# Kernel optimization log

Measured on AMD Instinct MI355X. Metric: run time of the kernel, lower is better.

Reference implementation:

```python
import jax, jax.numpy as jnp
import numpy as np

N_NODES = 100000
N_EDGES = 3200000
FEAT = 32
N_ITER = 6  # -> n_iter - 1 = 5 SimpleConv layers
MIN_VAL, MAX_VAL = 0.0, 2.0


def setup_inputs() -> dict:
    key = jax.random.key(0)
    k = jax.random.split(key, 6)
    return {
        "x": jax.random.uniform(k[0], (N_NODES, FEAT), dtype=jnp.float32) * 2.0,
        "edge_index": jax.random.randint(k[1], (2, N_EDGES), 0, N_NODES, dtype=jnp.int32),
        "edge_mask": jax.random.randint(k[2], (N_EDGES,), 0, 2, dtype=jnp.int32),
        "edge_scale": jax.random.uniform(k[3], (N_EDGES,), dtype=jnp.float32),
        "pert_mask": jax.random.uniform(k[4], (N_EDGES,), dtype=jnp.float32),
        "edge_weight": jax.random.uniform(k[5], (N_EDGES,), dtype=jnp.float32),
    }


def reference(x, edge_index, edge_mask, edge_scale, pert_mask, edge_weight):
    # edge_index *= edge_mask (masked edges collapse to node 0, as in the torch code)
    ei = edge_index * edge_mask.astype(edge_index.dtype)  # [2, E]
    src, dst = ei[0], ei[1]
    # edge_weight = (edge_weight * (1 - pert_mask) + pert_mask) * edge_scale
    w = (edge_weight * (1.0 - pert_mask) + pert_mask) * edge_scale  # [E]

    def step(x, _):
        # SimpleConv(aggr='sum'): out[dst] += w_e * x[src]
        msgs = x[src] * w[:, None]                                   # [E, F]
        x_new = jax.ops.segment_sum(msgs, dst, num_segments=N_NODES)  # [N, F]
        # max_update: x + Hardtanh(-1,1)(x_new - x)
        x_new = x + jnp.clip(x_new - x, -1.0, 1.0)
        # act: Hardtanh(min_val, max_val)
        return jnp.clip(x_new, MIN_VAL, MAX_VAL), None

    x, _ = jax.lax.scan(step, x, None, length=N_ITER - 1)
    return x
```

## Files before the change

### kernel.cpp

```cpp
#include <hip/hip_runtime.h>
#include <hip/hip_fp16.h>

#define NNODES 100000
#define NEDGES 3200000
#define FEAT 32
#define NITER 5
#define NF (NNODES * FEAT)

#define BUCK_SH 8
#define BUCK_SZ 256
#define NBK 391
#define CHUNKF 4096
#define NBF 782
#define NT (NBF * NBK)
#define NTB 299

__global__ void ws_kernel(const int* __restrict__ edge_index,
                          const int* __restrict__ edge_mask,
                          const float* __restrict__ edge_scale,
                          const float* __restrict__ pert_mask,
                          const float* __restrict__ edge_weight,
                          int2* __restrict__ pay,
                          unsigned short* __restrict__ bkt,
                          int* __restrict__ M,
                          float* __restrict__ S_part) {
    __shared__ int h[NBK];
    __shared__ float sred[256];
    const int b = blockIdx.x;
    for (int k = threadIdx.x; k < NBK; k += 256) h[k] = 0;
    __syncthreads();
    const int base = b * CHUNKF;
    float ms = 0.0f;
    for (int it = 0; it < CHUNKF / 256; ++it) {
        const int e = base + it * 256 + threadIdx.x;
        if (e < NEDGES) {
            const int m = edge_mask[e];
            const float w = (edge_weight[e] * (1.0f - pert_mask[e]) + pert_mask[e]) * edge_scale[e];
            const int src = edge_index[e];
            const int dst = edge_index[NEDGES + e];
            pay[e] = make_int2(src | ((dst & (BUCK_SZ - 1)) << 20), __float_as_int(w));
            if (m) {
                bkt[e] = (unsigned short)(dst >> BUCK_SH);
                atomicAdd(&h[dst >> BUCK_SH], 1);
            } else {
                bkt[e] = (unsigned short)0xFFFFu;
                ms += w;
            }
        }
    }
    sred[threadIdx.x] = ms;
    __syncthreads();
    for (int off = 128; off; off >>= 1) {
        if (threadIdx.x < off) sred[threadIdx.x] += sred[threadIdx.x + off];
        __syncthreads();
    }
    if (threadIdx.x == 0) S_part[b] = sred[0];
    for (int k = threadIdx.x; k < NBK; k += 256) M[b * NBK + k] = h[k];
}

__global__ void sreduce_kernel(const float* __restrict__ S_part, float* __restrict__ S) {
    __shared__ float s[1024];
    float a = 0.0f;
    for (int i = threadIdx.x; i < NBF; i += 1024) a += S_part[i];
    s[threadIdx.x] = a;
    __syncthreads();
    for (int off = 512; off; off >>= 1) {
        if (threadIdx.x < off) s[threadIdx.x] += s[threadIdx.x + off];
        __syncthreads();
    }
    if (threadIdx.x == 0) *S = s[0];
}

__global__ void tscan1_kernel(const int* __restrict__ M, int* __restrict__ tb) {
    __shared__ int s[1024];
    const int i = blockIdx.x * 1024 + threadIdx.x;
    int v = 0;
    if (i < NT) v = M[(i % NBF) * NBK + (i / NBF)];
    s[threadIdx.x] = v;
    __syncthreads();
    for (int off = 512; off; off >>= 1) {
        if (threadIdx.x < off) s[threadIdx.x] += s[threadIdx.x + off];
        __syncthreads();
    }
    if (threadIdx.x == 0) tb[blockIdx.x] = s[0];
}

__global__ void tscan2_kernel(const int* __restrict__ tb, int* __restrict__ tboff,
                              int* __restrict__ bucket_base) {
    __shared__ int s[512];
    const int tid = threadIdx.x;
    int v = (tid < NTB) ? tb[tid] : 0;
    s[tid] = v;
    __syncthreads();
    for (int off = 1; off < 512; off <<= 1) {
        int t = (tid >= off) ? s[tid - off] : 0;
        __syncthreads();
        s[tid] += t;
        __syncthreads();
    }
    if (tid < NTB) tboff[tid] = s[tid] - v;
    if (tid == 511) bucket_base[NBK] = s[511];
}

__global__ void tscan3_kernel(const int* __restrict__ M, const int* __restrict__ tboff,
                              int* __restrict__ scanT, int* __restrict__ bucket_base) {
    __shared__ int s[1024];
    const int tid = threadIdx.x;
    const int i = blockIdx.x * 1024 + tid;
    int v = 0;
    if (i < NT) v = M[(i % NBF) * NBK + (i / NBF)];
    s[tid] = v;
    __syncthreads();
    for (int off = 1; off < 1024; off <<= 1) {
        int t = (tid >= off) ? s[tid - off] : 0;
        __syncthreads();
        s[tid] += t;
        __syncthreads();
    }
    if (i < NT) {
        const int excl = tboff[blockIdx.x] + s[tid] - v;
        scanT[i] = excl;
        if (i % NBF == 0) bucket_base[i / NBF] = excl;
    }
}

__global__ void fill782_kernel(const int2* __restrict__ pay,
                               const unsigned short* __restrict__ bkt,
                               const int* __restrict__ scanT,
                               int2* __restrict__ e8tmp) {
    __shared__ int off[NBK];
    const int b = blockIdx.x;
    for (int k = threadIdx.x; k < NBK; k += 256) off[k] = scanT[k * NBF + b];
    __syncthreads();
    const int base = b * CHUNKF;
    for (int it = 0; it < CHUNKF / 256; ++it) {
        const int e = base + it * 256 + threadIdx.x;
        if (e < NEDGES) {
            const unsigned short k = bkt[e];
            if (k != 0xFFFFu) {
                const int pos = atomicAdd(&off[k], 1);
                e8tmp[pos] = pay[e];
            }
        }
    }
}

__global__ void bsort_kernel(const int2* __restrict__ e8tmp,
                             const int* __restrict__ bucket_base,
                             unsigned* __restrict__ e4,
                             int* __restrict__ row_ptr) {
    __shared__ int h[BUCK_SZ];
    __shared__ int s[BUCK_SZ];
    __shared__ int woff[BUCK_SZ];
    const int k = blockIdx.x;
    const int tid = threadIdx.x;
    const int base0 = bucket_base[k];
    const int cnt = bucket_base[k + 1] - base0;
    h[tid] = 0;
    __syncthreads();
    for (int i = tid; i < cnt; i += 256) {
        const int dstl = e8tmp[base0 + i].x >> 20;
        atomicAdd(&h[dstl], 1);
    }
    __syncthreads();
    s[tid] = h[tid];
    __syncthreads();
    for (int off = 1; off < BUCK_SZ; off <<= 1) {
        int t = (tid >= off) ? s[tid - off] : 0;
        __syncthreads();
        s[tid] += t;
        __syncthreads();
    }
    {
        const int excl = s[tid] - h[tid];
        const int d = k * BUCK_SZ + tid;
        if (d < NNODES) row_ptr[d] = base0 + excl;
        woff[tid] = excl;
    }
    if (k == NBK - 1 && tid == 0) row_ptr[NNODES] = bucket_base[NBK];
    __syncthreads();
    for (int i = tid; i < cnt; i += 256) {
        const int2 v = e8tmp[base0 + i];
        const int dstl = v.x >> 20;
        const unsigned src = (unsigned)(v.x & 0xFFFFF);
        __half hw = __float2half_rn(__int_as_float(v.y));
        const unsigned h16 = (unsigned)(*reinterpret_cast<unsigned short*>(&hw)) & 0x7FFFu;
        const int pos = atomicAdd(&woff[dstl], 1);
        e4[base0 + pos] = (src << 15) | h16;
    }
}

__global__ void cvt_kernel(const float* __restrict__ x, __half* __restrict__ xh) {
    const int i = blockIdx.x * 256 + threadIdx.x;
    const float4 v = reinterpret_cast<const float4*>(x)[i];
    const int node = i >> 3;
    const int q = i & 7;
    const int fh = q >> 2;
    const int part = q & 3;
    __half2 h01 = __floats2half2_rn(v.x, v.y);
    __half2 h23 = __floats2half2_rn(v.z, v.w);
    *reinterpret_cast<uint2*>((char*)xh + (size_t)fh * (NNODES * 32) + node * 32 + part * 8)
        = make_uint2(*(unsigned*)&h01, *(unsigned*)&h23);
}

__global__ void gather_kernel(const __half* __restrict__ xh,
                              const int* __restrict__ row_ptr,
                              const unsigned* __restrict__ e4,
                              const float* __restrict__ S,
                              float* __restrict__ out,
                              __half* __restrict__ outh) {
    const int bid = blockIdx.x;
    const int r = bid & 7;
    const int fh = r >> 2;
    const int blk = (bid >> 3) * 4 + (r & 3);
    if (blk >= 6250) return;
    const int lane = threadIdx.x & 63;
    const int wid = threadIdx.x >> 6;
    const int nq   = lane >> 4;
    const int slot = (lane >> 1) & 7;
    const int part = lane & 1;
    const int node = blk * 16 + wid * 4 + nq;
    const int beg = row_ptr[node];
    const int end = row_ptr[node + 1];
    const char* xhc = (const char*)xh + (size_t)fh * (NNODES * 32);

    float a0=0.f,a1=0.f,a2=0.f,a3=0.f,a4=0.f,a5=0.f,a6=0.f,a7=0.f;
    const int em1c = (end - 1 > beg) ? (end - 1) : beg;
    for (int i = beg + slot; __any(i < end); i += 8) {
        const bool valid = (i < end);
        const unsigned v = e4[valid ? i : em1c];
        unsigned short w16 = (unsigned short)(v & 0x7FFFu);
        const float wv = __half2float(*reinterpret_cast<const __half*>(&w16));
        const float w = valid ? wv : 0.0f;
        const uint4 hv = *reinterpret_cast<const uint4*>(
            xhc + (size_t)((v >> 10) & 0xFFFFE0u) + (part << 4));
        float2 f;
        f = __half22float2(*(const __half2*)&hv.x); a0 = fmaf(w, f.x, a0); a1 = fmaf(w, f.y, a1);
        f = __half22float2(*(const __half2*)&hv.y); a2 = fmaf(w, f.x, a2); a3 = fmaf(w, f.y, a3);
        f = __half22float2(*(const __half2*)&hv.z); a4 = fmaf(w, f.x, a4); a5 = fmaf(w, f.y, a5);
        f = __half22float2(*(const __half2*)&hv.w); a6 = fmaf(w, f.x, a6); a7 = fmaf(w, f.y, a7);
    }
    #pragma unroll
    for (int off = 2; off <= 8; off <<= 1) {
        a0 += __shfl_xor(a0, off); a1 += __shfl_xor(a1, off);
        a2 += __shfl_xor(a2, off); a3 += __shfl_xor(a3, off);
        a4 += __shfl_xor(a4, off); a5 += __shfl_xor(a5, off);
        a6 += __shfl_xor(a6, off); a7 += __shfl_xor(a7, off);
    }
    if ((lane & 14) == 0) {
        const uint4 hx = *reinterpret_cast<const uint4*>(xhc + node * 32 + (part << 4));
        float2 f;
        f = __half22float2(*(const __half2*)&hx.x); const float x0f = f.x, x1f = f.y;
        f = __half22float2(*(const __half2*)&hx.y); const float x2f = f.x, x3f = f.y;
        f = __half22float2(*(const __half2*)&hx.z); const float x4f = f.x, x5f = f.y;
        f = __half22float2(*(const __half2*)&hx.w); const float x6f = f.x, x7f = f.y;
        if (node == 0) {
            const float S0 = *S;
            a0 = fmaf(S0, x0f, a0); a1 = fmaf(S0, x1f, a1);
            a2 = fmaf(S0, x2f, a2); a3 = fmaf(S0, x3f, a3);
            a4 = fmaf(S0, x4f, a4); a5 = fmaf(S0, x5f, a5);
            a6 = fmaf(S0, x6f, a6); a7 = fmaf(S0, x7f, a7);
        }
        const float r0 = fminf(fmaxf(x0f + fminf(fmaxf(a0 - x0f, -1.f), 1.f), 0.f), 2.f);
        const float r1 = fminf(fmaxf(x1f + fminf(fmaxf(a1 - x1f, -1.f), 1.f), 0.f), 2.f);
        const float r2 = fminf(fmaxf(x2f + fminf(fmaxf(a2 - x2f, -1.f), 1.f), 0.f), 2.f);
        const float r3 = fminf(fmaxf(x3f + fminf(fmaxf(a3 - x3f, -1.f), 1.f), 0.f), 2.f);
        const float r4 = fminf(fmaxf(x4f + fminf(fmaxf(a4 - x4f, -1.f), 1.f), 0.f), 2.f);
        const float r5 = fminf(fmaxf(x5f + fminf(fmaxf(a5 - x5f, -1.f), 1.f), 0.f), 2.f);
        const float r6 = fminf(fmaxf(x6f + fminf(fmaxf(a6 - x6f, -1.f), 1.f), 0.f), 2.f);
        const float r7 = fminf(fmaxf(x7f + fminf(fmaxf(a7 - x7f, -1.f), 1.f), 0.f), 2.f);
        __half2 h0 = __floats2half2_rn(r0, r1);
        __half2 h1 = __floats2half2_rn(r2, r3);
        __half2 h2 = __floats2half2_rn(r4, r5);
        __half2 h3 = __floats2half2_rn(r6, r7);
        uint4 hh;
        hh.x = *(unsigned*)&h0; hh.y = *(unsigned*)&h1;
        hh.z = *(unsigned*)&h2; hh.w = *(unsigned*)&h3;
        *reinterpret_cast<uint4*>((char*)outh + (size_t)fh * (NNODES * 32)
                                  + node * 32 + (part << 4)) = hh;
        if (out) {
            float* op = out + node * FEAT + (fh << 4) + (part << 3);
            *reinterpret_cast<float4*>(op)     = make_float4(r0, r1, r2, r3);
            *reinterpret_cast<float4*>(op + 4) = make_float4(r4, r5, r6, r7);
        }
    }
}

extern "C" void kernel_launch(void* const* d_in, const int* in_sizes, int n_in,
                              void* d_out, int out_size, void* d_ws, size_t ws_size,
                              hipStream_t stream) {
    const float* x0         = (const float*)d_in[0];
    const int*   edge_index = (const int*)d_in[1];
    const int*   edge_mask  = (const int*)d_in[2];
    const float* edge_scale = (const float*)d_in[3];
    const float* pert_mask  = (const float*)d_in[4];
    const float* edge_weight= (const float*)d_in[5];
    float* xout = (float*)d_out;

    char* ws = (char*)d_ws;
    float* S        = (float*)(ws);
    float* S_part   = (float*)(ws + 1024);
    int*   tb       = (int*)(ws + 64 * 1024);
    int*   tboff    = (int*)(ws + 68 * 1024);
    int*   bbase    = (int*)(ws + 72 * 1024);
    int*   row_ptr  = (int*)(ws + 80 * 1024);
    int*   M        = (int*)(ws + 1  * 1024 * 1024);
    int*   scanT    = (int*)(ws + 3  * 1024 * 1024);
    int2*  e8tmp    = (int2*)(ws + 5  * 1024 * 1024);
    unsigned* e4    = (unsigned*)(ws + 18 * 1024 * 1024);
    int2*  pay      = (int2*)(ws + 25 * 1024 * 1024);
    unsigned short* bkt = (unsigned short*)(ws + 51 * 1024 * 1024);
    __half* xh0     = (__half*)(ws + 25 * 1024 * 1024);
    __half* xh1     = (__half*)(ws + 32 * 1024 * 1024);

    ws_kernel<<<NBF, 256, 0, stream>>>(edge_index, edge_mask, edge_scale,
                                       pert_mask, edge_weight, pay, bkt, M, S_part);
    sreduce_kernel<<<1, 1024, 0, stream>>>(S_part, S);
    tscan1_kernel<<<NTB, 1024, 0, stream>>>(M, tb);
    tscan2_kernel<<<1, 512, 0, stream>>>(tb, tboff, bbase);
    tscan3_kernel<<<NTB, 1024, 0, stream>>>(M, tboff, scanT, bbase);
    fill782_kernel<<<NBF, 256, 0, stream>>>(pay, bkt, scanT, e8tmp);
    bsort_kernel<<<NBK, 256, 0, stream>>>(e8tmp, bbase, e4, row_ptr);
    cvt_kernel<<<NF / 4 / 256, 256, 0, stream>>>(x0, xh0);

    const int gblocks = 12504;
    __half* xhb[2] = { xh0, xh1 };
    for (int it = 0; it < NITER; ++it) {
        gather_kernel<<<gblocks, 256, 0, stream>>>(xhb[it & 1], row_ptr, e4, S,
                                                   (it == NITER - 1) ? xout : nullptr,
                                                   xhb[(it + 1) & 1]);
    }
}
```

Before: 219.6 us.

## Split half-precision features into four 8-feature planes, one 16-byte gather per edge

The fp16 feature copy changes from two 16-feature planes (32 bytes per node) to four 8-feature planes (16 bytes per node). Each gather block now handles one quarter of the features, and each lane loads a single 16-byte row per edge. Each feature plane is 1.6 MB instead of 3.2 MB, so the randomly gathered working set per block is smaller and more cache-friendly. In exchange, every edge index and weight is read four times instead of twice, and nodes are split into two halves per block group.

Result: slower. 257.7 us (+17.3%).

```diff
diff --git a/kernel.cpp b/kernel.cpp
--- a/kernel.cpp
+++ b/kernel.cpp
@@ -194,12 +194,12 @@
     const int i = blockIdx.x * 256 + threadIdx.x;
     const float4 v = reinterpret_cast<const float4*>(x)[i];
     const int node = i >> 3;
-    const int q = i & 7;
-    const int fh = q >> 2;
-    const int part = q & 3;
+    const int q8 = i & 7;
+    const int q = q8 >> 1;
+    const int part = q8 & 1;
     __half2 h01 = __floats2half2_rn(v.x, v.y);
     __half2 h23 = __floats2half2_rn(v.z, v.w);
-    *reinterpret_cast<uint2*>((char*)xh + (size_t)fh * (NNODES * 32) + node * 32 + part * 8)
+    *reinterpret_cast<uint2*>((char*)xh + (size_t)q * (NNODES * 16) + node * 16 + part * 8)
         = make_uint2(*(unsigned*)&h01, *(unsigned*)&h23);
 }
 
@@ -211,18 +211,19 @@
                               __half* __restrict__ outh) {
     const int bid = blockIdx.x;
     const int r = bid & 7;
-    const int fh = r >> 2;
-    const int blk = (bid >> 3) * 4 + (r & 3);
-    if (blk >= 6250) return;
+    const int q = r >> 1;
+    const int hs = r & 1;
+    const int blkl = bid >> 3;
     const int lane = threadIdx.x & 63;
     const int wid = threadIdx.x >> 6;
-    const int nq   = lane >> 4;
-    const int slot = (lane >> 1) & 7;
-    const int part = lane & 1;
-    const int node = blk * 16 + wid * 4 + nq;
+    const int nq   = lane >> 3;
+    const int slot = lane & 7;
+    const int lid = blkl * 32 + wid * 8 + nq;
+    if (lid >= 50000) return;
+    const int node = hs * 50000 + lid;
     const int beg = row_ptr[node];
     const int end = row_ptr[node + 1];
-    const char* xhc = (const char*)xh + (size_t)fh * (NNODES * 32);
+    const char* xhc = (const char*)xh + (size_t)q * (NNODES * 16);
 
     float a0=0.f,a1=0.f,a2=0.f,a3=0.f,a4=0.f,a5=0.f,a6=0.f,a7=0.f;
     const int em1c = (end - 1 > beg) ? (end - 1) : beg;
@@ -233,7 +234,7 @@
         const float wv = __half2float(*reinterpret_cast<const __half*>(&w16));
         const float w = valid ? wv : 0.0f;
         const uint4 hv = *reinterpret_cast<const uint4*>(
-            xhc + (size_t)((v >> 10) & 0xFFFFE0u) + (part << 4));
+            xhc + (size_t)((v >> 11) & 0xFFFFF0u));
         float2 f;
         f = __half22float2(*(const __half2*)&hv.x); a0 = fmaf(w, f.x, a0); a1 = fmaf(w, f.y, a1);
         f = __half22float2(*(const __half2*)&hv.y); a2 = fmaf(w, f.x, a2); a3 = fmaf(w, f.y, a3);
@@ -241,14 +242,14 @@
         f = __half22float2(*(const __half2*)&hv.w); a6 = fmaf(w, f.x, a6); a7 = fmaf(w, f.y, a7);
     }
     #pragma unroll
-    for (int off = 2; off <= 8; off <<= 1) {
+    for (int off = 1; off <= 4; off <<= 1) {
         a0 += __shfl_xor(a0, off); a1 += __shfl_xor(a1, off);
         a2 += __shfl_xor(a2, off); a3 += __shfl_xor(a3, off);
         a4 += __shfl_xor(a4, off); a5 += __shfl_xor(a5, off);
         a6 += __shfl_xor(a6, off); a7 += __shfl_xor(a7, off);
     }
-    if ((lane & 14) == 0) {
-        const uint4 hx = *reinterpret_cast<const uint4*>(xhc + node * 32 + (part << 4));
+    if ((lane & 7) == 0) {
+        const uint4 hx = *reinterpret_cast<const uint4*>(xhc + node * 16);
         float2 f;
         f = __half22float2(*(const __half2*)&hx.x); const float x0f = f.x, x1f = f.y;
         f = __half22float2(*(const __half2*)&hx.y); const float x2f = f.x, x3f = f.y;
@@ -276,10 +277,9 @@
         uint4 hh;
         hh.x = *(unsigned*)&h0; hh.y = *(unsigned*)&h1;
         hh.z = *(unsigned*)&h2; hh.w = *(unsigned*)&h3;
-        *reinterpret_cast<uint4*>((char*)outh + (size_t)fh * (NNODES * 32)
-                                  + node * 32 + (part << 4)) = hh;
+        *reinterpret_cast<uint4*>((char*)outh + (size_t)q * (NNODES * 16) + node * 16) = hh;
         if (out) {
-            float* op = out + node * FEAT + (fh << 4) + (part << 3);
+            float* op = out + node * FEAT + (q << 3);
             *reinterpret_cast<float4*>(op)     = make_float4(r0, r1, r2, r3);
             *reinterpret_cast<float4*>(op + 4) = make_float4(r4, r5, r6, r7);
         }
```
